# Performance work log

Measured on AMD Instinct MI355X. Metric: run time of the kernel, lower is better.

Reference implementation:

```python
import jax, jax.numpy as jnp
import numpy as np

PS = 7   # spatial patch size
PT = 2   # temporal patch size


def setup_inputs() -> dict:
    key = jax.random.key(0)
    T, C, H, W = 10, 3, 512, 512
    Q = 262144
    k1, k2, k3, k4 = jax.random.split(key, 4)
    vid2fill = jnp.zeros((T, C, H, W), dtype=jnp.float32)
    patches = jax.random.normal(k1, (Q, PT, C, PS, PS), dtype=jnp.float32)
    # in-range top-left anchors (t, h, w)
    t = jax.random.randint(k2, (Q,), 0, T - PT + 1)
    h = jax.random.randint(k3, (Q,), 0, H - PS + 1)
    w = jax.random.randint(k4, (Q,), 0, W - PS + 1)
    queryInds = jnp.stack([t, h, w], axis=-1).astype(jnp.int32)
    return {"vid2fill": vid2fill, "patches": patches, "queryInds": queryInds}


def reference(vid2fill, patches, queryInds):
    # vid2fill: [T,C,H,W]; patches: [Q,pt,C,ps,ps]; queryInds: [Q,3] (t,h,w)
    T, C, H, W = vid2fill.shape
    Q, pt, _, ps, _ = patches.shape
    dt = jnp.arange(pt)[:, None, None]          # [pt,1,1]
    di = jnp.arange(ps)[None, :, None]          # [1,ps,1]
    dj = jnp.arange(ps)[None, None, :]          # [1,1,ps]
    t = queryInds[:, 0][:, None, None, None] + dt   # [Q,pt,ps,ps] (broadcast)
    h = queryInds[:, 1][:, None, None, None] + di
    w = queryInds[:, 2][:, None, None, None] + dj
    flat = (t * H + h) * W + w                  # [Q,pt,ps,ps] flat pixel index
    # scatter-add patches (channels-last) into flattened video buffer
    vid_flat = jnp.transpose(vid2fill, (0, 2, 3, 1)).reshape(T * H * W, C)
    p = jnp.transpose(patches, (0, 1, 3, 4, 2)).reshape(-1, C)  # [Q*pt*ps*ps, C]
    out = vid_flat.at[flat.reshape(-1)].add(p)
    return jnp.transpose(out.reshape(T, H, W, C), (0, 3, 1, 2))
```

## Files before the change

### kernel.cpp

```cpp
#include <hip/hip_runtime.h>

constexpr int T_DIM = 10, C_DIM = 3, H_DIM = 512, W_DIM = 512;
constexpr int PT = 2, PS = 7;
constexpr int ELEM_PER_Q = PT * C_DIM * PS * PS;
constexpr int HALF      = C_DIM * PS * PS;
constexpr int TILE = 38;
constexpr int NBH = 14, NBW = 14;
constexpr int NTB = T_DIM - PT + 1;
constexpr int NBINS = NTB * NBH * NBW;
constexpr int BINPAD = 2048;
constexpr int HTILE = TILE + PS - 1;
constexpr int ACC_SLICE = C_DIM * HTILE * HTILE;
constexpr int NPAIR = T_DIM / 2;


__global__ __launch_bounds__(256) void ScatterNL_hist(
    const int* __restrict__ qinds, int Q, int* __restrict__ counts)
{
    __shared__ int hloc[NBINS];
    for (int i = threadIdx.x; i < NBINS; i += blockDim.x) hloc[i] = 0;
    __syncthreads();
    int stride = gridDim.x * blockDim.x;
    for (int q = blockIdx.x * blockDim.x + threadIdx.x; q < Q; q += stride) {
        int t = qinds[3*q], h = qinds[3*q+1], w = qinds[3*q+2];
        int b = (t * NBH + h / TILE) * NBW + w / TILE;
        atomicAdd(&hloc[b], 1);
    }
    __syncthreads();
    for (int i = threadIdx.x; i < NBINS; i += blockDim.x)
        if (hloc[i]) atomicAdd(&counts[i], hloc[i]);
}

__global__ __launch_bounds__(256) void ScatterNL_scan(
    const int* __restrict__ counts, int* __restrict__ offsets,
    int* __restrict__ cursors)
{
    __shared__ int buf[2][256];
    int tid = threadIdx.x;
    int base = tid * 7;
    int loc[7];
    int s = 0;
    #pragma unroll
    for (int i = 0; i < 7; ++i) {
        int b = base + i;
        int v = (b < NBINS) ? counts[b] : 0;
        loc[i] = s;
        s += v;
    }
    buf[0][tid] = s;
    __syncthreads();
    int src = 0;
    for (int d = 1; d < 256; d <<= 1) {
        int x = buf[src][tid] + ((tid >= d) ? buf[src][tid - d] : 0);
        buf[src ^ 1][tid] = x;
        __syncthreads();
        src ^= 1;
    }
    int excl = (tid == 0) ? 0 : buf[src][tid - 1];
    #pragma unroll
    for (int i = 0; i < 7; ++i) {
        int b = base + i;
        if (b < NBINS) {
            offsets[b] = excl + loc[i];
            cursors[b] = excl + loc[i];
        }
    }
    if (tid == 255) offsets[NBINS] = buf[src][255];
}

__global__ __launch_bounds__(256) void ScatterNL_fill(
    const int* __restrict__ qinds, int Q, int* __restrict__ cursors,
    int* __restrict__ list)
{
    int stride = gridDim.x * blockDim.x;
    for (int q = blockIdx.x * blockDim.x + threadIdx.x; q < Q; q += stride) {
        int t = qinds[3*q], h = qinds[3*q+1], w = qinds[3*q+2];
        int sh = h / TILE, sw = w / TILE;
        int b = (t * NBH + sh) * NBW + sw;
        int pos = atomicAdd(&cursors[b], 1);
        list[pos] = q | ((h - sh * TILE) << 18) | ((w - sw * TILE) << 24);
    }
}

__global__ __launch_bounds__(256) void ScatterNL_copy(
    const float* __restrict__ vid, float* __restrict__ out, int n4)
{
    int stride = gridDim.x * blockDim.x;
    const float4* src = (const float4*)vid;
    float4* dst = (float4*)out;
    for (int i = blockIdx.x * blockDim.x + threadIdx.x; i < n4; i += stride)
        dst[i] = src[i];
}

__global__ __launch_bounds__(512, 6) void ScatterNL_accum(
    const float* __restrict__ patches, const int* __restrict__ offsets,
    const int* __restrict__ list, float* __restrict__ out)
{
    __shared__ float acc[2 * ACC_SLICE];

    int bid = blockIdx.x;
    int k   = bid / (NBH * NBW);
    int r   = bid % (NBH * NBW);
    int bh  = r / NBW, bw = r % NBW;
    int h0  = bh * TILE, w0 = bw * TILE;

    for (int i = threadIdx.x; i < 2 * ACC_SLICE; i += blockDim.x)
        acc[i] = 0.f;
    __syncthreads();

    const int lane = threadIdx.x & 63;
    const int wv   = threadIdx.x >> 6;
    int off3[3];
    #pragma unroll
    for (int s = 0; s < 3; ++s) {
        int kx = lane + 64 * s;
        int kk = (kx < HALF) ? kx : 0;
        int c = kk / 49, rr = kk % 49;
        off3[s] = (c * HTILE + rr / 7) * HTILE + rr % 7;
    }
    const bool v2ok = (lane < HALF - 128);
    int offf[5], slf[5];
    #pragma unroll
    for (int s = 0; s < 5; ++s) {
        int kx = lane + 64 * s;
        int kk = (kx < ELEM_PER_Q) ? kx : 0;
        slf[s] = kk / HALF;
        int rem = kk % HALF;
        int c = rem / 49, rr = rem % 49;
        offf[s] = slf[s] * ACC_SLICE + (c * HTILE + rr / 7) * HTILE + rr % 7;
    }
    const bool v4ok = (lane < ELEM_PER_Q - 256);

    auto procHalf = [&](int bin, int dtOff, int ss) {
        int start = offsets[bin], n = offsets[bin + 1] - start;
        int sbase = ss * ACC_SLICE;
        for (int base = wv * 4; base < n; base += 32) {
            int i0 = start + base;
            int nb = n - base;
            int e0 = list[i0];
            int e1 = (nb > 1) ? list[i0 + 1] : e0;
            int e2 = (nb > 2) ? list[i0 + 2] : e0;
            int e3 = (nb > 3) ? list[i0 + 3] : e0;
            const float* B0 = patches + (size_t)(e0 & 0x3FFFF) * ELEM_PER_Q + dtOff;
            const float* B1 = patches + (size_t)(e1 & 0x3FFFF) * ELEM_PER_Q + dtOff;
            const float* B2 = patches + (size_t)(e2 & 0x3FFFF) * ELEM_PER_Q + dtOff;
            const float* B3 = patches + (size_t)(e3 & 0x3FFFF) * ELEM_PER_Q + dtOff;
            float a00 = B0[lane], a01 = B0[lane+64], a02 = v2ok ? B0[lane+128] : 0.f;
            float a10 = B1[lane], a11 = B1[lane+64], a12 = v2ok ? B1[lane+128] : 0.f;
            float a20 = B2[lane], a21 = B2[lane+64], a22 = v2ok ? B2[lane+128] : 0.f;
            float a30 = B3[lane], a31 = B3[lane+64], a32 = v2ok ? B3[lane+128] : 0.f;
            __builtin_amdgcn_sched_barrier(0);
            int d0 = sbase + ((e0 >> 18) & 63) * HTILE + ((e0 >> 24) & 63);
            int d1 = sbase + ((e1 >> 18) & 63) * HTILE + ((e1 >> 24) & 63);
            int d2 = sbase + ((e2 >> 18) & 63) * HTILE + ((e2 >> 24) & 63);
            int d3 = sbase + ((e3 >> 18) & 63) * HTILE + ((e3 >> 24) & 63);
            atomicAdd(&acc[d0 + off3[0]], a00);
            atomicAdd(&acc[d0 + off3[1]], a01);
            if (v2ok) atomicAdd(&acc[d0 + off3[2]], a02);
            if (nb > 1) {
                atomicAdd(&acc[d1 + off3[0]], a10);
                atomicAdd(&acc[d1 + off3[1]], a11);
                if (v2ok) atomicAdd(&acc[d1 + off3[2]], a12);
            }
            if (nb > 2) {
                atomicAdd(&acc[d2 + off3[0]], a20);
                atomicAdd(&acc[d2 + off3[1]], a21);
                if (v2ok) atomicAdd(&acc[d2 + off3[2]], a22);
            }
            if (nb > 3) {
                atomicAdd(&acc[d3 + off3[0]], a30);
                atomicAdd(&acc[d3 + off3[1]], a31);
                if (v2ok) atomicAdd(&acc[d3 + off3[2]], a32);
            }
        }
    };

    {
        int bin = (2 * k * NBH + bh) * NBW + bw;
        int start = offsets[bin], n = offsets[bin + 1] - start;
        for (int base = wv * 2; base < n; base += 16) {
            int i0 = start + base;
            int nb = n - base;
            int e0 = list[i0];
            int e1 = (nb > 1) ? list[i0 + 1] : e0;
            const float* B0 = patches + (size_t)(e0 & 0x3FFFF) * ELEM_PER_Q;
            const float* B1 = patches + (size_t)(e1 & 0x3FFFF) * ELEM_PER_Q;
            float a0[5], a1[5];
            #pragma unroll
            for (int s = 0; s < 5; ++s) {
                bool v = (s < 4) || v4ok;
                a0[s] = v ? B0[lane + 64*s] : 0.f;
                a1[s] = v ? B1[lane + 64*s] : 0.f;
            }
            __builtin_amdgcn_sched_barrier(0);
            int d0 = ((e0 >> 18) & 63) * HTILE + ((e0 >> 24) & 63);
            int d1 = ((e1 >> 18) & 63) * HTILE + ((e1 >> 24) & 63);
            #pragma unroll
            for (int s = 0; s < 5; ++s)
                if ((s < 4) || v4ok) atomicAdd(&acc[d0 + offf[s]], a0[s]);
            if (nb > 1) {
                #pragma unroll
                for (int s = 0; s < 5; ++s)
                    if ((s < 4) || v4ok) atomicAdd(&acc[d1 + offf[s]], a1[s]);
            }
        }
    }
    if (2 * k + 1 <= T_DIM - PT)
        procHalf(((2 * k + 1) * NBH + bh) * NBW + bw, 0, 1);
    if (2 * k - 1 >= 0)
        procHalf(((2 * k - 1) * NBH + bh) * NBW + bw, HALF, 0);

    __syncthreads();

    int He = min(HTILE, H_DIM - h0);
    int We = min(HTILE, W_DIM - w0);
    for (int ls = 0; ls < 2; ++ls) {
        int ts = 2 * k + ls;
        #pragma unroll
        for (int c = 0; c < C_DIM; ++c) {
            for (int y = wv; y < He; y += 8) {
                if (lane < We) {
                    float v = acc[(ls * C_DIM + c) * HTILE * HTILE + y * HTILE + lane];
                    size_t o = (((size_t)ts * C_DIM + c) * H_DIM + (h0 + y)) * W_DIM + w0 + lane;
                    atomicAdd(&out[o], v);
                }
            }
        }
    }
}

extern "C" void kernel_launch(void* const* d_in, const int* in_sizes, int n_in,
                              void* d_out, int out_size, void* d_ws, size_t ws_size,
                              hipStream_t stream) {
    const float* vid     = (const float*)d_in[0];
    const float* patches = (const float*)d_in[1];
    const int*   qinds   = (const int*)d_in[2];
    float* out = (float*)d_out;
    int Q = in_sizes[2] / 3;

    int* ws      = (int*)d_ws;
    int* counts  = ws;
    int* offsets = ws + BINPAD;
    int* cursors = ws + 2 * BINPAD;
    int* list    = ws + 3 * BINPAD;

    hipMemsetAsync(counts, 0, BINPAD * sizeof(int), stream);
    ScatterNL_copy<<<1024, 256, 0, stream>>>(vid, out,
        T_DIM * C_DIM * H_DIM * W_DIM / 4);
    ScatterNL_hist<<<256, 256, 0, stream>>>(qinds, Q, counts);
    ScatterNL_scan<<<1, 256, 0, stream>>>(counts, offsets, cursors);
    ScatterNL_fill<<<256, 256, 0, stream>>>(qinds, Q, cursors, list);
    ScatterNL_accum<<<NPAIR * NBH * NBW, 512, 0, stream>>>(
        patches, offsets, list, out);
}
```

Measured before the change: 847.2 us.

## Physically reorder patches into bin order before tile accumulation

Adds a pass that copies each patch into a workspace buffer at its sorted bin position, using a 304-float stride and storing the in-tile offset in the padding. The accumulate kernel then reads patches contiguously per bin instead of gathering through an index list. This aims to replace scattered patch reads with streaming ones, at the cost of an extra full read and write of the roughly 300 MB patch array. The old list-based path remains as a fallback when the workspace is too small.

```diff
diff --git a/kernel.cpp b/kernel.cpp
--- a/kernel.cpp
+++ b/kernel.cpp
@@ -12,6 +12,7 @@
 constexpr int HTILE = TILE + PS - 1;
 constexpr int ACC_SLICE = C_DIM * HTILE * HTILE;
 constexpr int NPAIR = T_DIM / 2;
+constexpr int STRIDE_F = 304;
 
 
 __global__ __launch_bounds__(256) void ScatterNL_hist(
@@ -68,7 +69,205 @@
     if (tid == 255) offsets[NBINS] = buf[src][255];
 }
 
-__global__ __launch_bounds__(256) void ScatterNL_fill(
+__global__ __launch_bounds__(256) void ScatterNL_fillPos(
+    const int* __restrict__ qinds, int Q, int* __restrict__ cursors,
+    int* __restrict__ posOf)
+{
+    int stride = gridDim.x * blockDim.x;
+    for (int q = blockIdx.x * blockDim.x + threadIdx.x; q < Q; q += stride) {
+        int t = qinds[3*q], h = qinds[3*q+1], w = qinds[3*q+2];
+        int b = (t * NBH + h / TILE) * NBW + w / TILE;
+        posOf[q] = atomicAdd(&cursors[b], 1);
+    }
+}
+
+__global__ __launch_bounds__(256) void ScatterNL_reorder(
+    const float* __restrict__ patches, const int* __restrict__ qinds,
+    const int* __restrict__ posOf, int Q, float* __restrict__ reord)
+{
+    int gw   = (blockIdx.x * blockDim.x + threadIdx.x) >> 6;
+    int lane = threadIdx.x & 63;
+    int nw   = (gridDim.x * blockDim.x) >> 6;
+    const bool tail = (lane < ELEM_PER_Q - 256);
+    for (int q0 = 2 * gw; q0 < Q; q0 += 2 * nw) {
+        bool two = (q0 + 1 < Q);
+        int p0 = posOf[q0];
+        int p1 = two ? posOf[q0 + 1] : p0;
+        int h0 = qinds[3*q0+1], w0 = qinds[3*q0+2];
+        int h1 = two ? qinds[3*q0+4] : 0, w1 = two ? qinds[3*q0+5] : 0;
+        const float* s0 = patches + (size_t)q0 * ELEM_PER_Q;
+        const float* s1 = s0 + ELEM_PER_Q;
+        float a0 = s0[lane], a1 = s0[lane+64], a2 = s0[lane+128], a3 = s0[lane+192];
+        float a4 = tail ? s0[lane+256] : 0.f;
+        float b0 = 0.f, b1 = 0.f, b2 = 0.f, b3 = 0.f, b4 = 0.f;
+        if (two) {
+            b0 = s1[lane]; b1 = s1[lane+64]; b2 = s1[lane+128]; b3 = s1[lane+192];
+            b4 = tail ? s1[lane+256] : 0.f;
+        }
+        __builtin_amdgcn_sched_barrier(0);
+        float* d0 = reord + (size_t)p0 * STRIDE_F;
+        d0[lane] = a0; d0[lane+64] = a1; d0[lane+128] = a2; d0[lane+192] = a3;
+        if (tail) d0[lane+256] = a4;
+        if (lane == 0)
+            d0[294] = __int_as_float((h0 % TILE) | ((w0 % TILE) << 6));
+        if (two) {
+            float* d1 = reord + (size_t)p1 * STRIDE_F;
+            d1[lane] = b0; d1[lane+64] = b1; d1[lane+128] = b2; d1[lane+192] = b3;
+            if (tail) d1[lane+256] = b4;
+            if (lane == 0)
+                d1[294] = __int_as_float((h1 % TILE) | ((w1 % TILE) << 6));
+        }
+    }
+}
+
+__global__ __launch_bounds__(256) void ScatterNL_copy(
+    const float* __restrict__ vid, float* __restrict__ out, int n4)
+{
+    int stride = gridDim.x * blockDim.x;
+    const float4* src = (const float4*)vid;
+    float4* dst = (float4*)out;
+    for (int i = blockIdx.x * blockDim.x + threadIdx.x; i < n4; i += stride)
+        dst[i] = src[i];
+}
+
+__global__ __launch_bounds__(512, 6) void ScatterNL_accum2(
+    const float* __restrict__ reord, const int* __restrict__ offsets,
+    float* __restrict__ out)
+{
+    __shared__ float acc[2 * ACC_SLICE];
+
+    int bid = blockIdx.x;
+    int k   = bid / (NBH * NBW);
+    int r   = bid % (NBH * NBW);
+    int bh  = r / NBW, bw = r % NBW;
+    int h0  = bh * TILE, w0 = bw * TILE;
+
+    for (int i = threadIdx.x; i < 2 * ACC_SLICE; i += blockDim.x)
+        acc[i] = 0.f;
+    __syncthreads();
+
+    const int lane = threadIdx.x & 63;
+    const int wv   = threadIdx.x >> 6;
+
+    int off3[3];
+    #pragma unroll
+    for (int s = 0; s < 3; ++s) {
+        int kx = lane + 64 * s;
+        int kk = (kx < HALF) ? kx : 0;
+        int c = kk / 49, rr = kk % 49;
+        off3[s] = (c * HTILE + rr / 7) * HTILE + rr % 7;
+    }
+    const bool v2ok = (lane < HALF - 128);
+    int offf[5];
+    #pragma unroll
+    for (int s = 0; s < 5; ++s) {
+        int kx = lane + 64 * s;
+        int kk = (kx < ELEM_PER_Q) ? kx : 0;
+        int sl = kk / HALF;
+        int rem = kk % HALF;
+        int c = rem / 49, rr = rem % 49;
+        offf[s] = sl * ACC_SLICE + (c * HTILE + rr / 7) * HTILE + rr % 7;
+    }
+    const bool v4ok = (lane < ELEM_PER_Q - 256);
+
+    {
+        int bin = (2 * k * NBH + bh) * NBW + bw;
+        int start = offsets[bin], n = offsets[bin + 1] - start;
+        for (int base = wv * 2; base < n; base += 16) {
+            int nb = n - base;
+            const float* P0 = reord + (size_t)(start + base) * STRIDE_F;
+            const float* P1 = (nb > 1) ? P0 + STRIDE_F : P0;
+            float a0[5], a1[5];
+            #pragma unroll
+            for (int s = 0; s < 5; ++s) {
+                bool v = (s < 4) || v4ok;
+                a0[s] = v ? P0[lane + 64*s] : 0.f;
+                a1[s] = v ? P1[lane + 64*s] : 0.f;
+            }
+            int m0 = __float_as_int(P0[294]);
+            int m1 = __float_as_int(P1[294]);
+            __builtin_amdgcn_sched_barrier(0);
+            int d0 = (m0 & 63) * HTILE + ((m0 >> 6) & 63);
+            int d1 = (m1 & 63) * HTILE + ((m1 >> 6) & 63);
+            #pragma unroll
+            for (int s = 0; s < 5; ++s)
+                if ((s < 4) || v4ok) atomicAdd(&acc[d0 + offf[s]], a0[s]);
+            if (nb > 1) {
+                #pragma unroll
+                for (int s = 0; s < 5; ++s)
+                    if ((s < 4) || v4ok) atomicAdd(&acc[d1 + offf[s]], a1[s]);
+            }
+        }
+    }
+
+    auto procHalf = [&](int bin, int dtOff, int ss) {
+        int start = offsets[bin], n = offsets[bin + 1] - start;
+        int sbase = ss * ACC_SLICE;
+        for (int base = wv * 4; base < n; base += 32) {
+            int nb = n - base;
+            const float* P0 = reord + (size_t)(start + base) * STRIDE_F;
+            const float* P1 = (nb > 1) ? P0 + STRIDE_F     : P0;
+            const float* P2 = (nb > 2) ? P0 + 2*STRIDE_F   : P0;
+            const float* P3 = (nb > 3) ? P0 + 3*STRIDE_F   : P0;
+            float a00 = P0[dtOff+lane], a01 = P0[dtOff+lane+64], a02 = v2ok ? P0[dtOff+lane+128] : 0.f;
+            float a10 = P1[dtOff+lane], a11 = P1[dtOff+lane+64], a12 = v2ok ? P1[dtOff+lane+128] : 0.f;
+            float a20 = P2[dtOff+lane], a21 = P2[dtOff+lane+64], a22 = v2ok ? P2[dtOff+lane+128] : 0.f;
+            float a30 = P3[dtOff+lane], a31 = P3[dtOff+lane+64], a32 = v2ok ? P3[dtOff+lane+128] : 0.f;
+            int m0 = __float_as_int(P0[294]);
+            int m1 = __float_as_int(P1[294]);
+            int m2 = __float_as_int(P2[294]);
+            int m3 = __float_as_int(P3[294]);
+            __builtin_amdgcn_sched_barrier(0);
+            int d0 = sbase + (m0 & 63) * HTILE + ((m0 >> 6) & 63);
+            int d1 = sbase + (m1 & 63) * HTILE + ((m1 >> 6) & 63);
+            int d2 = sbase + (m2 & 63) * HTILE + ((m2 >> 6) & 63);
+            int d3 = sbase + (m3 & 63) * HTILE + ((m3 >> 6) & 63);
+            atomicAdd(&acc[d0 + off3[0]], a00);
+            atomicAdd(&acc[d0 + off3[1]], a01);
+            if (v2ok) atomicAdd(&acc[d0 + off3[2]], a02);
+            if (nb > 1) {
+                atomicAdd(&acc[d1 + off3[0]], a10);
+                atomicAdd(&acc[d1 + off3[1]], a11);
+                if (v2ok) atomicAdd(&acc[d1 + off3[2]], a12);
+            }
+            if (nb > 2) {
+                atomicAdd(&acc[d2 + off3[0]], a20);
+                atomicAdd(&acc[d2 + off3[1]], a21);
+                if (v2ok) atomicAdd(&acc[d2 + off3[2]], a22);
+            }
+            if (nb > 3) {
+                atomicAdd(&acc[d3 + off3[0]], a30);
+                atomicAdd(&acc[d3 + off3[1]], a31);
+                if (v2ok) atomicAdd(&acc[d3 + off3[2]], a32);
+            }
+        }
+    };
+    if (2 * k + 1 <= T_DIM - PT)
+        procHalf(((2 * k + 1) * NBH + bh) * NBW + bw, 0, 1);
+    if (2 * k - 1 >= 0)
+        procHalf(((2 * k - 1) * NBH + bh) * NBW + bw, HALF, 0);
+
+    __syncthreads();
+
+    int He = min(HTILE, H_DIM - h0);
+    int We = min(HTILE, W_DIM - w0);
+    for (int ls = 0; ls < 2; ++ls) {
+        int ts = 2 * k + ls;
+        #pragma unroll
+        for (int c = 0; c < C_DIM; ++c) {
+            for (int y = wv; y < He; y += 8) {
+                if (lane < We) {
+                    float v = acc[(ls * C_DIM + c) * HTILE * HTILE + y * HTILE + lane];
+                    size_t o = (((size_t)ts * C_DIM + c) * H_DIM + (h0 + y)) * W_DIM + w0 + lane;
+                    atomicAdd(&out[o], v);
+                }
+            }
+        }
+    }
+}
+
+
+__global__ __launch_bounds__(256) void ScatterNL_fillList(
     const int* __restrict__ qinds, int Q, int* __restrict__ cursors,
     int* __restrict__ list)
 {
@@ -82,32 +281,18 @@
     }
 }
 
-__global__ __launch_bounds__(256) void ScatterNL_copy(
-    const float* __restrict__ vid, float* __restrict__ out, int n4)
-{
-    int stride = gridDim.x * blockDim.x;
-    const float4* src = (const float4*)vid;
-    float4* dst = (float4*)out;
-    for (int i = blockIdx.x * blockDim.x + threadIdx.x; i < n4; i += stride)
-        dst[i] = src[i];
-}
-
-__global__ __launch_bounds__(512, 6) void ScatterNL_accum(
+__global__ __launch_bounds__(512, 6) void ScatterNL_accumList(
     const float* __restrict__ patches, const int* __restrict__ offsets,
     const int* __restrict__ list, float* __restrict__ out)
 {
     __shared__ float acc[2 * ACC_SLICE];
-
     int bid = blockIdx.x;
     int k   = bid / (NBH * NBW);
     int r   = bid % (NBH * NBW);
     int bh  = r / NBW, bw = r % NBW;
     int h0  = bh * TILE, w0 = bw * TILE;
-
-    for (int i = threadIdx.x; i < 2 * ACC_SLICE; i += blockDim.x)
-        acc[i] = 0.f;
-    __syncthreads();
-
+    for (int i = threadIdx.x; i < 2 * ACC_SLICE; i += blockDim.x) acc[i] = 0.f;
+    __syncthreads();
     const int lane = threadIdx.x & 63;
     const int wv   = threadIdx.x >> 6;
     int off3[3];
@@ -119,18 +304,17 @@
         off3[s] = (c * HTILE + rr / 7) * HTILE + rr % 7;
     }
     const bool v2ok = (lane < HALF - 128);
-    int offf[5], slf[5];
+    int offf[5];
     #pragma unroll
     for (int s = 0; s < 5; ++s) {
         int kx = lane + 64 * s;
         int kk = (kx < ELEM_PER_Q) ? kx : 0;
-        slf[s] = kk / HALF;
+        int sl = kk / HALF;
         int rem = kk % HALF;
         int c = rem / 49, rr = rem % 49;
-        offf[s] = slf[s] * ACC_SLICE + (c * HTILE + rr / 7) * HTILE + rr % 7;
+        offf[s] = sl * ACC_SLICE + (c * HTILE + rr / 7) * HTILE + rr % 7;
     }
     const bool v4ok = (lane < ELEM_PER_Q - 256);
-
     auto procHalf = [&](int bin, int dtOff, int ss) {
         int start = offsets[bin], n = offsets[bin + 1] - start;
         int sbase = ss * ACC_SLICE;
@@ -174,7 +358,6 @@
             }
         }
     };
-
     {
         int bin = (2 * k * NBH + bh) * NBW + bw;
         int start = offsets[bin], n = offsets[bin + 1] - start;
@@ -209,9 +392,7 @@
         procHalf(((2 * k + 1) * NBH + bh) * NBW + bw, 0, 1);
     if (2 * k - 1 >= 0)
         procHalf(((2 * k - 1) * NBH + bh) * NBW + bw, HALF, 0);
-
-    __syncthreads();
-
+    __syncthreads();
     int He = min(HTILE, H_DIM - h0);
     int We = min(HTILE, W_DIM - w0);
     for (int ls = 0; ls < 2; ++ls) {
@@ -242,14 +423,26 @@
     int* counts  = ws;
     int* offsets = ws + BINPAD;
     int* cursors = ws + 2 * BINPAD;
-    int* list    = ws + 3 * BINPAD;
+    int* slot    = ws + 3 * BINPAD;
+
+    size_t metaBytes = ((size_t)(3 * BINPAD) + (size_t)Q) * sizeof(int);
+    size_t reordOff  = (metaBytes + 255) & ~(size_t)255;
+    size_t need      = reordOff + (size_t)Q * STRIDE_F * sizeof(float);
 
     hipMemsetAsync(counts, 0, BINPAD * sizeof(int), stream);
     ScatterNL_copy<<<1024, 256, 0, stream>>>(vid, out,
         T_DIM * C_DIM * H_DIM * W_DIM / 4);
     ScatterNL_hist<<<256, 256, 0, stream>>>(qinds, Q, counts);
     ScatterNL_scan<<<1, 256, 0, stream>>>(counts, offsets, cursors);
-    ScatterNL_fill<<<256, 256, 0, stream>>>(qinds, Q, cursors, list);
-    ScatterNL_accum<<<NPAIR * NBH * NBW, 512, 0, stream>>>(
-        patches, offsets, list, out);
-}
+
+    if (ws_size >= need) {
+        float* reord = (float*)((char*)d_ws + reordOff);
+        ScatterNL_fillPos<<<256, 256, 0, stream>>>(qinds, Q, cursors, slot);
+        ScatterNL_reorder<<<2048, 256, 0, stream>>>(patches, qinds, slot, Q, reord);
+        ScatterNL_accum2<<<NPAIR * NBH * NBW, 512, 0, stream>>>(reord, offsets, out);
+    } else {
+        ScatterNL_fillList<<<256, 256, 0, stream>>>(qinds, Q, cursors, slot);
+        ScatterNL_accumList<<<NPAIR * NBH * NBW, 512, 0, stream>>>(
+            patches, offsets, slot, out);
+    }
+}
```

Measured after the change: 1.004 ms. 18.5% more time.

## Reorder patches by row cell and gather-accumulate in registers instead of LDS atomics

Applied to the files above, without the earlier changes.

Adds a finer binning by (tile, row) cell, physically reorders patch data into a sorted padded buffer with packed offsets, and replaces the LDS-atomic scatter with a gather kernel. In that kernel each thread owns output pixels, keeps register accumulators, and walks only the relevant row cells from a double-buffered LDS staging area. The goal is to remove LDS atomic contention and scattered patch reads. In exchange it adds an extra full copy of the patch data (about 300MB written and read), a serial single-block scan over about 67K cells, and extra kernel launches. The old path is kept as a fallback when the workspace is too small.

```diff
diff --git a/kernel.cpp b/kernel.cpp
--- a/kernel.cpp
+++ b/kernel.cpp
@@ -12,6 +12,242 @@
 constexpr int HTILE = TILE + PS - 1;
 constexpr int ACC_SLICE = C_DIM * HTILE * HTILE;
 constexpr int NPAIR = T_DIM / 2;
+constexpr int STRIDE_F = 304;
+constexpr int NCELL = NBINS * TILE;
+constexpr int CELLPAD = 67136;
+
+
+
+__global__ __launch_bounds__(256) void ScatterNL_hist2(
+    const int* __restrict__ qinds, int Q, int* __restrict__ counts2)
+{
+    int stride = gridDim.x * blockDim.x;
+    for (int q = blockIdx.x * blockDim.x + threadIdx.x; q < Q; q += stride) {
+        int t = qinds[3*q], h = qinds[3*q+1], w = qinds[3*q+2];
+        int sh = h / TILE, sw = w / TILE;
+        int cell = ((t * NBH + sh) * NBW + sw) * TILE + (h - sh * TILE);
+        atomicAdd(&counts2[cell], 1);
+    }
+}
+
+__global__ __launch_bounds__(256) void ScatterNL_scan2(
+    const int* __restrict__ counts2, int* __restrict__ offsets2,
+    int* __restrict__ cursors2)
+{
+    constexpr int CPB = 262;
+    __shared__ int buf[2][256];
+    int tid = threadIdx.x;
+    int base = tid * CPB;
+    int s = 0;
+    for (int i = 0; i < CPB; ++i) {
+        int b = base + i;
+        s += (b < NCELL) ? counts2[b] : 0;
+    }
+    buf[0][tid] = s;
+    __syncthreads();
+    int src = 0;
+    for (int d = 1; d < 256; d <<= 1) {
+        int x = buf[src][tid] + ((tid >= d) ? buf[src][tid - d] : 0);
+        buf[src ^ 1][tid] = x;
+        __syncthreads();
+        src ^= 1;
+    }
+    int run = (tid == 0) ? 0 : buf[src][tid - 1];
+    for (int i = 0; i < CPB; ++i) {
+        int b = base + i;
+        if (b < NCELL) {
+            int v = counts2[b];
+            offsets2[b] = run;
+            cursors2[b] = run;
+            run += v;
+        }
+    }
+    if (tid == 255) offsets2[NCELL] = run;
+}
+
+__global__ __launch_bounds__(256) void ScatterNL_fillPos2(
+    const int* __restrict__ qinds, int Q, int* __restrict__ cursors2,
+    int* __restrict__ posOf)
+{
+    int stride = gridDim.x * blockDim.x;
+    for (int q = blockIdx.x * blockDim.x + threadIdx.x; q < Q; q += stride) {
+        int t = qinds[3*q], h = qinds[3*q+1], w = qinds[3*q+2];
+        int sh = h / TILE, sw = w / TILE;
+        int cell = ((t * NBH + sh) * NBW + sw) * TILE + (h - sh * TILE);
+        posOf[q] = atomicAdd(&cursors2[cell], 1);
+    }
+}
+
+__global__ __launch_bounds__(256) void ScatterNL_reorder(
+    const float* __restrict__ patches, const int* __restrict__ qinds,
+    const int* __restrict__ posOf, int Q, float* __restrict__ reord)
+{
+    int gw   = (blockIdx.x * blockDim.x + threadIdx.x) >> 6;
+    int lane = threadIdx.x & 63;
+    int nw   = (gridDim.x * blockDim.x) >> 6;
+    const bool tail = (lane < ELEM_PER_Q - 256);
+    for (int q0 = 2 * gw; q0 < Q; q0 += 2 * nw) {
+        bool two = (q0 + 1 < Q);
+        int p0 = posOf[q0];
+        int p1 = two ? posOf[q0 + 1] : p0;
+        int h0 = qinds[3*q0+1], w0 = qinds[3*q0+2];
+        int h1 = two ? qinds[3*q0+4] : 0, w1 = two ? qinds[3*q0+5] : 0;
+        const float* s0 = patches + (size_t)q0 * ELEM_PER_Q;
+        const float* s1 = s0 + ELEM_PER_Q;
+        float a0 = s0[lane], a1 = s0[lane+64], a2 = s0[lane+128], a3 = s0[lane+192];
+        float a4 = tail ? s0[lane+256] : 0.f;
+        float b0 = 0.f, b1 = 0.f, b2 = 0.f, b3 = 0.f, b4 = 0.f;
+        if (two) {
+            b0 = s1[lane]; b1 = s1[lane+64]; b2 = s1[lane+128]; b3 = s1[lane+192];
+            b4 = tail ? s1[lane+256] : 0.f;
+        }
+        __builtin_amdgcn_sched_barrier(0);
+        float* d0 = reord + (size_t)p0 * STRIDE_F;
+        d0[lane] = a0; d0[lane+64] = a1; d0[lane+128] = a2; d0[lane+192] = a3;
+        if (tail) d0[lane+256] = a4;
+        if (lane == 0)
+            d0[294] = __int_as_float((h0 % TILE) | ((w0 % TILE) << 6));
+        if (two) {
+            float* d1 = reord + (size_t)p1 * STRIDE_F;
+            d1[lane] = b0; d1[lane+64] = b1; d1[lane+128] = b2; d1[lane+192] = b3;
+            if (tail) d1[lane+256] = b4;
+            if (lane == 0)
+                d1[294] = __int_as_float((h1 % TILE) | ((w1 % TILE) << 6));
+        }
+    }
+}
+
+__global__ __launch_bounds__(256) void ScatterNL_copy(
+    const float* __restrict__ vid, float* __restrict__ out, int n4)
+{
+    int stride = gridDim.x * blockDim.x;
+    const float4* src = (const float4*)vid;
+    float4* dst = (float4*)out;
+    for (int i = blockIdx.x * blockDim.x + threadIdx.x; i < n4; i += stride)
+        dst[i] = src[i];
+}
+
+__global__ __launch_bounds__(512) void ScatterNL_gather(
+    const float* __restrict__ reord, const int* __restrict__ offsets2,
+    const float* __restrict__ vid, float* __restrict__ out)
+{
+    constexpr int CHUNK = 32;
+    constexpr int SLOT  = 148;
+    __shared__ float stg[2][CHUNK * SLOT];
+    __shared__ int cellOff[TILE + 1];
+
+    int bid = blockIdx.x;
+    int k   = bid / (NBH * NBW);
+    int r   = bid % (NBH * NBW);
+    int bh  = r / NBW, bw = r % NBW;
+    int h0  = bh * TILE, w0 = bw * TILE;
+    int He  = min(HTILE, H_DIM - h0);
+    int We  = min(HTILE, W_DIM - w0);
+
+    const int lane = threadIdx.x & 63;
+    const int wv   = threadIdx.x >> 6;
+
+    float r4[4][3];
+
+    auto LOADS = [&](int c0, int E, int dtOff) {
+        #pragma unroll
+        for (int u = 0; u < 4; ++u) {
+            int g = c0 + wv * 4 + u;
+            if (g < E) {
+                const float* s = reord + (size_t)g * STRIDE_F + dtOff;
+                r4[u][0] = s[lane];
+                r4[u][1] = s[lane + 64];
+                r4[u][2] = (lane < 19) ? s[lane + 128]
+                         : (lane == 19) ? reord[(size_t)g * STRIDE_F + 294] : 0.f;
+            }
+        }
+        __builtin_amdgcn_sched_barrier(0);
+    };
+    auto WRITES = [&](int c0, int E, int b) {
+        #pragma unroll
+        for (int u = 0; u < 4; ++u) {
+            int g = c0 + wv * 4 + u;
+            if (g < E) {
+                float* d = &stg[b][(wv * 4 + u) * SLOT];
+                d[lane] = r4[u][0];
+                d[lane + 64] = r4[u][1];
+                if (lane < 19) d[lane + 128] = r4[u][2];
+                else if (lane == 19) d[147] = r4[u][2];
+            }
+        }
+    };
+
+    for (int sl = 0; sl < 2; ++sl) {
+        float acc[6][3];
+        #pragma unroll
+        for (int j = 0; j < 6; ++j) {
+            acc[j][0] = 0.f; acc[j][1] = 0.f; acc[j][2] = 0.f;
+        }
+
+        for (int si = 0; si < 2; ++si) {
+            int tb = (si == 0) ? 2 * k : (sl == 0 ? 2 * k - 1 : 2 * k + 1);
+            int dt = (si == 0) ? sl   : (sl == 0 ? 1 : 0);
+            if (tb < 0 || tb > T_DIM - PT) continue;
+            int bin = (tb * NBH + bh) * NBW + bw;
+            int dtOff = dt * HALF;
+
+            if (threadIdx.x < TILE + 1)
+                cellOff[threadIdx.x] = offsets2[bin * TILE + threadIdx.x];
+            __syncthreads();
+            int S = cellOff[0], E = cellOff[TILE];
+            if (S == E) continue;
+
+            LOADS(S, E, dtOff);
+            WRITES(S, E, 0);
+            __syncthreads();
+
+            int nb = 0;
+            for (int c0 = S; c0 < E; c0 += CHUNK, nb ^= 1) {
+                int c1 = min(c0 + CHUNK, E);
+                bool more = (c1 < E);
+                if (more) LOADS(c0 + CHUNK, E, dtOff);
+
+                const float* sb = stg[nb];
+                #pragma unroll
+                for (int j = 0; j < 6; ++j) {
+                    int y = wv + 8 * j;
+                    int loI = y - 6; if (loI < 0) loI = 0; if (loI > TILE) loI = TILE;
+                    int hiI = (y < TILE) ? y + 1 : TILE;
+                    int a = cellOff[loI]; if (a < c0) a = c0;
+                    int b2 = cellOff[hiI]; if (b2 > c1) b2 = c1;
+                    for (int g = a; g < b2; ++g) {
+                        int mb = (g - c0) * SLOT;
+                        int meta = __float_as_int(sb[mb + 147]);
+                        int dh = meta & 63, dw = (meta >> 6) & 63;
+                        int dy = y - dh;
+                        int dx = lane - dw;
+                        bool hit = ((unsigned)dx < 7u);
+                        int e = mb + dy * 7 + (hit ? dx : 0);
+                        float v0 = sb[e], v1 = sb[e + 49], v2 = sb[e + 98];
+                        if (hit) {
+                            acc[j][0] += v0; acc[j][1] += v1; acc[j][2] += v2;
+                        }
+                    }
+                }
+
+                if (more) WRITES(c0 + CHUNK, E, nb ^ 1);
+                __syncthreads();
+            }
+        }
+
+        int ts = 2 * k + sl;
+        #pragma unroll
+        for (int j = 0; j < 6; ++j) {
+            int y = wv + 8 * j;
+            if (y < He && lane < We) {
+                size_t o = (((size_t)ts * C_DIM) * H_DIM + (h0 + y)) * W_DIM + w0 + lane;
+                atomicAdd(&out[o], acc[j][0]);
+                atomicAdd(&out[o + (size_t)H_DIM * W_DIM], acc[j][1]);
+                atomicAdd(&out[o + 2 * (size_t)H_DIM * W_DIM], acc[j][2]);
+            }
+        }
+    }
+}
 
 
 __global__ __launch_bounds__(256) void ScatterNL_hist(
@@ -68,7 +304,7 @@
     if (tid == 255) offsets[NBINS] = buf[src][255];
 }
 
-__global__ __launch_bounds__(256) void ScatterNL_fill(
+__global__ __launch_bounds__(256) void ScatterNL_fillList(
     const int* __restrict__ qinds, int Q, int* __restrict__ cursors,
     int* __restrict__ list)
 {
@@ -82,32 +318,18 @@
     }
 }
 
-__global__ __launch_bounds__(256) void ScatterNL_copy(
-    const float* __restrict__ vid, float* __restrict__ out, int n4)
-{
-    int stride = gridDim.x * blockDim.x;
-    const float4* src = (const float4*)vid;
-    float4* dst = (float4*)out;
-    for (int i = blockIdx.x * blockDim.x + threadIdx.x; i < n4; i += stride)
-        dst[i] = src[i];
-}
-
-__global__ __launch_bounds__(512, 6) void ScatterNL_accum(
+__global__ __launch_bounds__(512, 6) void ScatterNL_accumList(
     const float* __restrict__ patches, const int* __restrict__ offsets,
     const int* __restrict__ list, float* __restrict__ out)
 {
     __shared__ float acc[2 * ACC_SLICE];
-
     int bid = blockIdx.x;
     int k   = bid / (NBH * NBW);
     int r   = bid % (NBH * NBW);
     int bh  = r / NBW, bw = r % NBW;
     int h0  = bh * TILE, w0 = bw * TILE;
-
-    for (int i = threadIdx.x; i < 2 * ACC_SLICE; i += blockDim.x)
-        acc[i] = 0.f;
-    __syncthreads();
-
+    for (int i = threadIdx.x; i < 2 * ACC_SLICE; i += blockDim.x) acc[i] = 0.f;
+    __syncthreads();
     const int lane = threadIdx.x & 63;
     const int wv   = threadIdx.x >> 6;
     int off3[3];
@@ -119,18 +341,17 @@
         off3[s] = (c * HTILE + rr / 7) * HTILE + rr % 7;
     }
     const bool v2ok = (lane < HALF - 128);
-    int offf[5], slf[5];
+    int offf[5];
     #pragma unroll
     for (int s = 0; s < 5; ++s) {
         int kx = lane + 64 * s;
         int kk = (kx < ELEM_PER_Q) ? kx : 0;
-        slf[s] = kk / HALF;
+        int sl = kk / HALF;
         int rem = kk % HALF;
         int c = rem / 49, rr = rem % 49;
-        offf[s] = slf[s] * ACC_SLICE + (c * HTILE + rr / 7) * HTILE + rr % 7;
+        offf[s] = sl * ACC_SLICE + (c * HTILE + rr / 7) * HTILE + rr % 7;
     }
     const bool v4ok = (lane < ELEM_PER_Q - 256);
-
     auto procHalf = [&](int bin, int dtOff, int ss) {
         int start = offsets[bin], n = offsets[bin + 1] - start;
         int sbase = ss * ACC_SLICE;
@@ -174,7 +395,6 @@
             }
         }
     };
-
     {
         int bin = (2 * k * NBH + bh) * NBW + bw;
         int start = offsets[bin], n = offsets[bin + 1] - start;
@@ -209,9 +429,7 @@
         procHalf(((2 * k + 1) * NBH + bh) * NBW + bw, 0, 1);
     if (2 * k - 1 >= 0)
         procHalf(((2 * k - 1) * NBH + bh) * NBW + bw, HALF, 0);
-
-    __syncthreads();
-
+    __syncthreads();
     int He = min(HTILE, H_DIM - h0);
     int We = min(HTILE, W_DIM - w0);
     for (int ls = 0; ls < 2; ++ls) {
@@ -238,18 +456,39 @@
     float* out = (float*)d_out;
     int Q = in_sizes[2] / 3;
 
-    int* ws      = (int*)d_ws;
-    int* counts  = ws;
-    int* offsets = ws + BINPAD;
-    int* cursors = ws + 2 * BINPAD;
-    int* list    = ws + 3 * BINPAD;
-
-    hipMemsetAsync(counts, 0, BINPAD * sizeof(int), stream);
+    int* ws = (int*)d_ws;
+
+    size_t metaInts = (size_t)(3 * CELLPAD) + (size_t)Q;
+    size_t reordOff = (metaInts * sizeof(int) + 255) & ~(size_t)255;
+    size_t need     = reordOff + (size_t)Q * STRIDE_F * sizeof(float);
+
     ScatterNL_copy<<<1024, 256, 0, stream>>>(vid, out,
         T_DIM * C_DIM * H_DIM * W_DIM / 4);
-    ScatterNL_hist<<<256, 256, 0, stream>>>(qinds, Q, counts);
-    ScatterNL_scan<<<1, 256, 0, stream>>>(counts, offsets, cursors);
-    ScatterNL_fill<<<256, 256, 0, stream>>>(qinds, Q, cursors, list);
-    ScatterNL_accum<<<NPAIR * NBH * NBW, 512, 0, stream>>>(
-        patches, offsets, list, out);
-}
+
+    if (ws_size >= need) {
+        int* counts2  = ws;
+        int* offsets2 = ws + CELLPAD;
+        int* cursors2 = ws + 2 * CELLPAD;
+        int* posOf    = ws + 3 * CELLPAD;
+        float* reord  = (float*)((char*)d_ws + reordOff);
+
+        hipMemsetAsync(counts2, 0, CELLPAD * sizeof(int), stream);
+        ScatterNL_hist2<<<256, 256, 0, stream>>>(qinds, Q, counts2);
+        ScatterNL_scan2<<<1, 256, 0, stream>>>(counts2, offsets2, cursors2);
+        ScatterNL_fillPos2<<<256, 256, 0, stream>>>(qinds, Q, cursors2, posOf);
+        ScatterNL_reorder<<<2048, 256, 0, stream>>>(patches, qinds, posOf, Q, reord);
+        ScatterNL_gather<<<NPAIR * NBH * NBW, 512, 0, stream>>>(
+            reord, offsets2, vid, out);
+    } else {
+        int* counts  = ws;
+        int* offsets = ws + BINPAD;
+        int* cursors = ws + 2 * BINPAD;
+        int* list    = ws + 3 * BINPAD;
+        hipMemsetAsync(counts, 0, BINPAD * sizeof(int), stream);
+        ScatterNL_hist<<<256, 256, 0, stream>>>(qinds, Q, counts);
+        ScatterNL_scan<<<1, 256, 0, stream>>>(counts, offsets, cursors);
+        ScatterNL_fillList<<<256, 256, 0, stream>>>(qinds, Q, cursors, list);
+        ScatterNL_accumList<<<NPAIR * NBH * NBW, 512, 0, stream>>>(
+            patches, offsets, list, out);
+    }
+}
```

Result: slower. 915.8 us (+8.1%).
